# Performance work log

Measured on AMD Instinct MI355X. Metric: run time of the kernel, lower is better.

Reference implementation:

```python
import jax, jax.numpy as jnp
import numpy as np

# dims: 64 graphs x 1024 nodes, 32768 edges/graph, 256 feats, 64 pools/graph
B, NPG, EPG, F, C = 64, 1024, 32768, 256, 64
N, E = B * NPG, B * EPG


def setup_inputs() -> dict:
    key = jax.random.key(0)
    k1, k2, k3, k4, k5 = jax.random.split(key, 5)
    x = jax.random.normal(k1, (N, F), jnp.float32)
    # within-graph edges (block structure, as in real batched graphs)
    src = jax.random.randint(k2, (B, EPG), 0, NPG, dtype=jnp.int32)
    dst = jax.random.randint(k3, (B, EPG), 0, NPG, dtype=jnp.int32)
    off = (jnp.arange(B, dtype=jnp.int32) * NPG)[:, None]
    edge_index = jnp.stack([(src + off).reshape(-1), (dst + off).reshape(-1)], 0)
    edge_weight = jax.random.uniform(k4, (E,), jnp.float32)
    batch = jnp.repeat(jnp.arange(B, dtype=jnp.int32), NPG)
    batch_ptr = jnp.arange(B + 1, dtype=jnp.int32) * NPG
    # pooling_net stand-in: linear d_feat -> num_pools
    W = jax.random.normal(k5, (F, C), jnp.float32) * 0.05
    b = jnp.zeros((C,), jnp.float32)
    return dict(x=x, edge_index=edge_index, edge_weight=edge_weight,
                batch=batch, batch_ptr=batch_ptr, W=W, b=b)


def reference(x, edge_index, edge_weight, batch, batch_ptr, W, b):
    num_batches = batch_ptr.shape[0] - 1
    Cp = W.shape[1]  # num_pools_per_graph
    logits = x @ W + b                       # pooling_net(x, edge_index)
    sm = jax.nn.softmax(logits, axis=-1)     # [N, C]
    c = jnp.argmax(sm, axis=-1)              # hard cluster per node [N]
    p = jnp.take_along_axis(sm, c[:, None], axis=-1)[:, 0]
    # straight-through nonzero value of s (==1.0 in forward value)
    v = 1.0 - jax.lax.stop_gradient(p) + p
    gcl = batch * Cp + c                     # global cluster id [N]
    K = num_batches * Cp
    # out = S^T x  -> segment reduce over nodes by global cluster
    out = jax.ops.segment_sum(v[:, None] * x, gcl, num_segments=K)  # [K, F]
    # out_adj = S^T A S  (block diagonal over graphs): per-edge scatter
    src, dst = edge_index[0], edge_index[1]
    ci, cj = c[src], c[dst]
    gb = batch[src]
    flat = gb * (Cp * Cp) + ci * Cp + cj
    contrib = edge_weight * v[src] * v[dst]
    out_adj = jax.ops.segment_sum(contrib, flat, num_segments=num_batches * Cp * Cp)
    # dense block-diagonal index set (torch returns coalesced nonzeros;
    # jit needs static shapes, so we enumerate all within-graph pool pairs)
    idx = jnp.arange(num_batches * Cp * Cp, dtype=jnp.int32)
    bb, rem = idx // (Cp * Cp), idx % (Cp * Cp)
    out_edge_index = jnp.stack([bb * Cp + rem // Cp, bb * Cp + rem % Cp], 0)
    # link_loss = ||A - S S^T||_F / E  via exact decomposition
    a2 = jnp.sum(edge_weight * edge_weight)
    ap = jnp.sum(jnp.where(gcl[src] == gcl[dst], contrib, 0.0))
    vs2 = jax.ops.segment_sum(v * v, gcl, num_segments=K)
    p2 = jnp.sum(vs2 * vs2)
    link_loss = jnp.sqrt(jnp.maximum(a2 - 2.0 * ap + p2, 0.0)) / edge_index.shape[1]
    batch_out = jnp.repeat(jnp.arange(num_batches, dtype=jnp.int32), Cp)
    batch_ptr_out = jnp.arange(num_batches + 1, dtype=jnp.int32) * Cp
    return (out, out_edge_index, out_adj, link_loss, jnp.float32(0.0),
            batch_out, batch_ptr_out)
```

## Files before the change

### kernel.cpp

```cpp
#include <hip/hip_runtime.h>
#include <cstdint>
#include <cstddef>

typedef __attribute__((ext_vector_type(8))) short short8;
typedef __attribute__((ext_vector_type(4))) float f32x4;

#define GLOAD_LDS16(gsrc, ldst) \
    __builtin_amdgcn_global_load_lds( \
        (const __attribute__((address_space(1))) void*)(gsrc), \
        (__attribute__((address_space(3))) void*)(ldst), 16, 0, 0)

namespace {
constexpr int kN    = 65536;
constexpr int kF    = 256;
constexpr int kC    = 64;
constexpr int kNPG  = 1024;
constexpr int kB    = 64;
constexpr int kE    = 2097152;
constexpr int kK    = kB * kC;

constexpr size_t OFF_OUT  = 0;
constexpr size_t OFF_EIDX = (size_t)kK * kF;
constexpr size_t OFF_ADJ  = OFF_EIDX + 2ull*kB*kC*kC;
constexpr size_t OFF_LL   = OFF_ADJ + (size_t)kB*kC*kC;
constexpr size_t OFF_Z    = OFF_LL + 1;
constexpr size_t OFF_BOUT = OFF_Z + 1;
constexpr size_t OFF_BPTR = OFF_BOUT + kK;

constexpr size_t WS_C    = 0;
constexpr size_t WS_V    = 262144;
constexpr size_t WS_VS2  = 524288;
constexpr size_t WS_A2   = 540672;
constexpr size_t WS_PERM = 544768;
constexpr size_t WS_STRT = 806912;
constexpr size_t WS_WPH  = 1048576;
constexpr size_t WS_WPL  = 1081344;
constexpr size_t WS_PADJ = 544768;

__device__ __forceinline__ unsigned short bf16_rn(float f)
{
    const unsigned int b = __float_as_uint(f);
    return (unsigned short)((b + 0x7fffu + ((b >> 16) & 1u)) >> 16);
}
}

__global__ __launch_bounds__(256) void k_const(float* __restrict__ out,
                                               const float* __restrict__ Wm,
                                               unsigned short* __restrict__ wph,
                                               unsigned short* __restrict__ wpl)
{
    const int i = blockIdx.x * 256 + threadIdx.x;
    constexpr int E2 = 2 * kB * kC * kC;
    constexpr int B3 = E2 + kK + kB + 1;
    if (i < E2) {
        const int half = i >= kB*kC*kC;
        const int idx  = half ? i - kB*kC*kC : i;
        const int bb = idx >> 12, rem = idx & 4095;
        const int val = half ? bb*kC + (rem & 63) : bb*kC + (rem >> 6);
        out[OFF_EIDX + i] = (float)val;
    } else if (i < E2 + kK) {
        const int j = i - E2;
        out[OFF_BOUT + j] = (float)(j >> 6);
    } else if (i < B3) {
        const int j = i - (E2 + kK);
        out[OFF_BPTR + j] = (float)(j * kC);
    } else if (i < B3 + 32768) {
        const int j  = (i - B3) & 16383;
        const int lo = (i - B3) >= 16384;
        const int jj = j & 7, lane = (j >> 3) & 63;
        const int nt = (j >> 9) & 3, ks = j >> 11;
        const float wv = Wm[(size_t)(ks*32 + (lane>>4)*8 + jj)*kC
                            + nt*16 + (lane & 15)];
        const unsigned short h = bf16_rn(wv);
        if (!lo) {
            wph[j] = h;
        } else {
            const float hf = __uint_as_float((unsigned int)h << 16);
            wpl[j] = bf16_rn(wv - hf);
        }
    }
}

__global__ __launch_bounds__(256) void k_logits(
    const float* __restrict__ x, const unsigned short* __restrict__ wph,
    const unsigned short* __restrict__ wpl, const float* __restrict__ bv,
    int* __restrict__ carr, float* __restrict__ varr)
{
    __shared__ float xs[2][128 * 32];
    const int tid  = threadIdx.x;
    const int lane = tid & 63;
    const int w    = tid >> 6;
    const int nbase = blockIdx.x * 128;
    const int l15  = lane & 15;
    const int kgrp = lane >> 4;

    const int snode = lane >> 3;
    const int sfo   = (((lane & 7) ^ snode)) * 4;

    f32x4 acc[2][4];
#pragma unroll
    for (int mt = 0; mt < 2; ++mt)
#pragma unroll
        for (int nt = 0; nt < 4; ++nt)
            acc[mt][nt] = f32x4{0.f, 0.f, 0.f, 0.f};

#pragma unroll
    for (int i = 0; i < 4; ++i) {
        const int g = w*4 + i;
        const float* src = x + (size_t)(nbase + g*8 + snode)*kF + sfo;
        GLOAD_LDS16(src, &xs[0][g*256]);
    }

#pragma unroll 1
    for (int c = 0; c < 8; ++c) {
        if (c < 7) {
#pragma unroll
            for (int i = 0; i < 4; ++i) {
                const int g = w*4 + i;
                const float* src = x + (size_t)(nbase + g*8 + snode)*kF
                                     + (c+1)*32 + sfo;
                GLOAD_LDS16(src, &xs[(c+1) & 1][g*256]);
            }
            asm volatile("s_waitcnt vmcnt(4)" ::: "memory");
        } else {
            asm volatile("s_waitcnt vmcnt(0)" ::: "memory");
        }
        __syncthreads();

        const float* __restrict__ xb = &xs[c & 1][0];
        short8 bh[4], bl[4];
#pragma unroll
        for (int nt = 0; nt < 4; ++nt) {
            const size_t wo = ((size_t)(c*4 + nt)*64 + lane) * 8;
            bh[nt] = *reinterpret_cast<const short8*>(wph + wo);
            bl[nt] = *reinterpret_cast<const short8*>(wpl + wo);
        }
#pragma unroll
        for (int mt = 0; mt < 2; ++mt) {
            const int row = w*32 + mt*16 + l15;
            const int sA  = ((kgrp*2)     ^ (row & 7)) * 4;
            const int sC  = ((kgrp*2 + 1) ^ (row & 7)) * 4;
            const float4 xa = *reinterpret_cast<const float4*>(
                &xb[row*32 + sA]);
            const float4 xc = *reinterpret_cast<const float4*>(
                &xb[row*32 + sC]);
            const float xv[8] = {xa.x, xa.y, xa.z, xa.w,
                                 xc.x, xc.y, xc.z, xc.w};
            short8 ah, al;
#pragma unroll
            for (int j = 0; j < 8; ++j) {
                const unsigned short h = bf16_rn(xv[j]);
                const float hf = __uint_as_float((unsigned int)h << 16);
                ah[j] = (short)h;
                al[j] = (short)bf16_rn(xv[j] - hf);
            }
#pragma unroll
            for (int nt = 0; nt < 4; ++nt) {
                acc[mt][nt] = __builtin_amdgcn_mfma_f32_16x16x32_bf16(
                    ah, bh[nt], acc[mt][nt], 0, 0, 0);
                acc[mt][nt] = __builtin_amdgcn_mfma_f32_16x16x32_bf16(
                    al, bh[nt], acc[mt][nt], 0, 0, 0);
                acc[mt][nt] = __builtin_amdgcn_mfma_f32_16x16x32_bf16(
                    ah, bl[nt], acc[mt][nt], 0, 0, 0);
                acc[mt][nt] = __builtin_amdgcn_mfma_f32_16x16x32_bf16(
                    al, bl[nt], acc[mt][nt], 0, 0, 0);
            }
        }
        __syncthreads();
    }

#pragma unroll
    for (int mt = 0; mt < 2; ++mt) {
#pragma unroll
        for (int nt = 0; nt < 4; ++nt) {
            const float b = bv[nt*16 + l15];
#pragma unroll
            for (int r = 0; r < 4; ++r) acc[mt][nt][r] += b;
        }
#pragma unroll
        for (int r = 0; r < 4; ++r) {
            float m = acc[mt][0][r]; int ci = l15;
#pragma unroll
            for (int nt = 1; nt < 4; ++nt) {
                if (acc[mt][nt][r] > m) { m = acc[mt][nt][r]; ci = nt*16 + l15; }
            }
#pragma unroll
            for (int off = 1; off < 16; off <<= 1) {
                const float om = __shfl_xor(m, off);
                const int   oc = __shfl_xor(ci, off);
                if (om > m || (om == m && oc < ci)) { m = om; ci = oc; }
            }
            float s = 0.f;
#pragma unroll
            for (int nt = 0; nt < 4; ++nt) s += expf(acc[mt][nt][r] - m);
#pragma unroll
            for (int off = 1; off < 16; off <<= 1) s += __shfl_xor(s, off);
            if (l15 == r) {
                const float p = 1.0f / s;
                const int n = nbase + w*32 + mt*16 + kgrp*4 + r;
                carr[n] = ci;
                varr[n] = (1.0f - p) + p;
            }
        }
    }
}

__global__ __launch_bounds__(1024) void k_sort(
    const int* __restrict__ carr, int* __restrict__ perm,
    int* __restrict__ startc)
{
    __shared__ int hist[16][64];
    __shared__ int startS[65];
    const int g = blockIdx.x;
    const int tid = threadIdx.x;
    const int w = tid >> 6, lane = tid & 63;
    const int c = carr[g*kNPG + tid];
    hist[tid >> 6][tid & 63] = 0;
    __syncthreads();
    unsigned long long mm = ~0ull;
#pragma unroll
    for (int b = 0; b < 6; ++b) {
        const unsigned long long bal = __ballot((c >> b) & 1);
        mm &= ((c >> b) & 1) ? bal : ~bal;
    }
    const unsigned long long ltmask =
        (lane == 0) ? 0ull : (~0ull >> (64 - lane));
    const int rank_in_wave = __popcll(mm & ltmask);
    const int leader = __ffsll((unsigned long long)mm) - 1;
    if (lane == leader) hist[w][c] = __popcll(mm);
    __syncthreads();
    if (w == 0) {
        int tot = 0;
#pragma unroll
        for (int i = 0; i < 16; ++i) tot += hist[i][lane];
        int pre = tot;
#pragma unroll
        for (int off = 1; off < 64; off <<= 1) {
            const int t = __shfl_up(pre, off);
            if (lane >= off) pre += t;
        }
        startS[lane + 1] = pre;
        if (lane == 0) startS[0] = 0;
    }
    __syncthreads();
    int before = startS[c];
    for (int i = 0; i < w; ++i) before += hist[i][c];
    perm[g*kNPG + before + rank_in_wave] = g*kNPG + tid;
    if (tid < 65) startc[g*65 + tid] = startS[tid];
}

__global__ __launch_bounds__(1024) void k_pool_x(
    const float* __restrict__ x, const int* __restrict__ perm,
    const int* __restrict__ startc, const float* __restrict__ varr,
    float* __restrict__ out, float* __restrict__ vs2)
{
    const int tid  = threadIdx.x;
    const int g    = blockIdx.x >> 3;
    const int fh   = blockIdx.x & 7;
    const int w    = tid >> 6;
    const int lane = tid & 63;
    const int q    = lane & 7;
    const int sub  = lane >> 3;
    const int fbase = fh*32 + q*4;
#pragma unroll
    for (int cc = 0; cc < 4; ++cc) {
        const int c = w*4 + cc;
        const int s = startc[g*65 + c];
        const int e = startc[g*65 + c + 1];
        float ax = 0.f, ay = 0.f, az = 0.f, aw = 0.f, v2 = 0.f;
        for (int base = s + sub; base < e; base += 8) {
            const int n = perm[(size_t)g*kNPG + base];
            const float v = varr[n];
            const float4 xv = *reinterpret_cast<const float4*>(
                x + (size_t)n*kF + fbase);
            ax = fmaf(v, xv.x, ax); ay = fmaf(v, xv.y, ay);
            az = fmaf(v, xv.z, az); aw = fmaf(v, xv.w, aw);
            v2 = fmaf(v, v, v2);
        }
#pragma unroll
        for (int off = 8; off < 64; off <<= 1) {
            ax += __shfl_xor(ax, off); ay += __shfl_xor(ay, off);
            az += __shfl_xor(az, off); aw += __shfl_xor(aw, off);
            v2 += __shfl_xor(v2, off);
        }
        if (sub == 0) {
            const float4 o = {ax, ay, az, aw};
            *reinterpret_cast<float4*>(
                out + OFF_OUT + (size_t)(g*kC + c)*kF + fbase) = o;
        }
        if (fh == 0 && lane == 0) vs2[g*kC + c] = v2;
    }
}

__global__ __launch_bounds__(1024) void k_adj(
    const int* __restrict__ ei, const float* __restrict__ ew,
    const int* __restrict__ carr, const float* __restrict__ varr,
    float* __restrict__ padj, float* __restrict__ a2p)
{
    __shared__ float adj[kC*kC];
    __shared__ float vls[kNPG];
    __shared__ int   cls[kNPG];
    __shared__ float wred[16];
    const int tid = threadIdx.x;
    const int bid = blockIdx.x;
    const int g   = bid >> 3;
    for (int i = tid; i < kC*kC; i += 1024) adj[i] = 0.f;
    vls[tid] = varr[g*kNPG + tid];
    cls[tid] = carr[g*kNPG + tid];
    __syncthreads();
    const int e0 = bid * 4096;
    float a2l = 0.f;
#pragma unroll
    for (int it = 0; it < 4; ++it) {
        const int e  = e0 + it*1024 + tid;
        const int sn = ei[e]      & (kNPG - 1);
        const int dn = ei[kE + e] & (kNPG - 1);
        const float wv = ew[e];
        a2l += wv * wv;
        atomicAdd(&adj[cls[sn]*kC + cls[dn]], wv * vls[sn] * vls[dn]);
    }
    __syncthreads();
#pragma unroll
    for (int r = 0; r < 4; ++r) {
        const int lin = r*1024 + tid;
        padj[(size_t)bid*4096 + lin] = adj[lin];
    }
#pragma unroll
    for (int off = 32; off > 0; off >>= 1) a2l += __shfl_down(a2l, off);
    if ((tid & 63) == 0) wred[tid >> 6] = a2l;
    __syncthreads();
    if (tid == 0) {
        float s = 0.f;
#pragma unroll
        for (int wv = 0; wv < 16; ++wv) s += wred[wv];
        a2p[bid] = s;
    }
}

__global__ __launch_bounds__(256) void k_adj_merge(
    const float* __restrict__ padj, float* __restrict__ out)
{
    const int id = blockIdx.x*256 + threadIdx.x;
    const int g = id >> 12, idx = id & 4095;
    float s = 0.f;
#pragma unroll
    for (int sp = 0; sp < 8; ++sp) s += padj[(size_t)(g*8 + sp)*4096 + idx];
    out[OFF_ADJ + id] = s;
}

__global__ __launch_bounds__(256) void k_final(
    const float* __restrict__ vs2, const float* __restrict__ a2p,
    float* __restrict__ out)
{
    const int tid = threadIdx.x;
    float p2l = 0.f, apl = 0.f;
#pragma unroll
    for (int r = 0; r < 16; ++r) {
        const int k = r*256 + tid;
        const float t = vs2[k];
        p2l += t*t;
        const int g = k >> 6, cc = k & 63;
        apl += out[OFF_ADJ + (size_t)g*4096 + cc*65];
    }
    float a2l = a2p[tid] + a2p[tid + 256];
#pragma unroll
    for (int off = 32; off > 0; off >>= 1) {
        p2l += __shfl_down(p2l, off);
        apl += __shfl_down(apl, off);
        a2l += __shfl_down(a2l, off);
    }
    __shared__ float red[3][4];
    if ((tid & 63) == 0) {
        red[0][tid>>6] = p2l; red[1][tid>>6] = apl; red[2][tid>>6] = a2l;
    }
    __syncthreads();
    if (tid == 0) {
        const float p2 = red[0][0]+red[0][1]+red[0][2]+red[0][3];
        const float ap = red[1][0]+red[1][1]+red[1][2]+red[1][3];
        const float a2 = red[2][0]+red[2][1]+red[2][2]+red[2][3];
        const float val = a2 - 2.0f*ap + p2;
        out[OFF_LL] = sqrtf(fmaxf(val, 0.f)) / (float)kE;
        out[OFF_Z]  = 0.0f;
    }
}

extern "C" void kernel_launch(void* const* d_in, const int* in_sizes, int n_in,
                              void* d_out, int out_size, void* d_ws, size_t ws_size,
                              hipStream_t stream)
{
    const float* x  = (const float*)d_in[0];
    const int*   ei = (const int*)d_in[1];
    const float* ew = (const float*)d_in[2];
    const float* Wm = (const float*)d_in[5];
    const float* bv = (const float*)d_in[6];
    float* out = (float*)d_out;
    char*  ws  = (char*)d_ws;
    int*   carr  = (int*)(ws + WS_C);
    float* varr  = (float*)(ws + WS_V);
    float* vs2   = (float*)(ws + WS_VS2);
    float* a2p   = (float*)(ws + WS_A2);
    int*   perm  = (int*)(ws + WS_PERM);
    int*   strt  = (int*)(ws + WS_STRT);
    unsigned short* wph = (unsigned short*)(ws + WS_WPH);
    unsigned short* wpl = (unsigned short*)(ws + WS_WPL);
    float* padj  = (float*)(ws + WS_PADJ);

    k_const    <<<2193, 256, 0, stream>>>(out, Wm, wph, wpl);
    k_logits   <<<512,  256, 0, stream>>>(x, wph, wpl, bv, carr, varr);
    k_sort     <<<64,  1024, 0, stream>>>(carr, perm, strt);
    k_pool_x   <<<512, 1024, 0, stream>>>(x, perm, strt, varr, out, vs2);
    k_adj      <<<512, 1024, 0, stream>>>(ei, ew, carr, varr, padj, a2p);
    k_adj_merge<<<1024, 256, 0, stream>>>(padj, out);
    k_final    <<<1,    256, 0, stream>>>(vs2, a2p, out);
}
```

Baseline: 75.55 us.

## Stage bf16 split weights in LDS and make logits tiles wave-private

The logits kernel now preloads the whole hi/lo bf16 weight matrix into shared memory once per block, instead of reading it from global memory every chunk. Each block handles 64 nodes, and each wave owns a private 16-row slice of the x tile, so the per-chunk block barriers are dropped and waits use only per-wave vmcnt. The grid doubles to 1024 blocks. The trade-off is about 80KB of LDS per block, which limits occupancy, plus a 64KB weight copy into LDS for every block.

```diff
diff --git a/kernel.cpp b/kernel.cpp
--- a/kernel.cpp
+++ b/kernel.cpp
@@ -86,121 +86,116 @@
     const unsigned short* __restrict__ wpl, const float* __restrict__ bv,
     int* __restrict__ carr, float* __restrict__ varr)
 {
-    __shared__ float xs[2][128 * 32];
+    __shared__ unsigned short wlds[32768];
+    __shared__ float xsl[2][64 * 32];
     const int tid  = threadIdx.x;
     const int lane = tid & 63;
     const int w    = tid >> 6;
-    const int nbase = blockIdx.x * 128;
+    const int nbase = blockIdx.x * 64;
     const int l15  = lane & 15;
     const int kgrp = lane >> 4;
 
     const int snode = lane >> 3;
-    const int sfo   = (((lane & 7) ^ snode)) * 4;
-
-    f32x4 acc[2][4];
-#pragma unroll
-    for (int mt = 0; mt < 2; ++mt)
-#pragma unroll
-        for (int nt = 0; nt < 4; ++nt)
-            acc[mt][nt] = f32x4{0.f, 0.f, 0.f, 0.f};
-
-#pragma unroll
-    for (int i = 0; i < 4; ++i) {
-        const int g = w*4 + i;
-        const float* src = x + (size_t)(nbase + g*8 + snode)*kF + sfo;
-        GLOAD_LDS16(src, &xs[0][g*256]);
-    }
+    const int sfo   = ((lane & 7) ^ snode) * 4;
+
+    f32x4 acc[4];
+#pragma unroll
+    for (int nt = 0; nt < 4; ++nt) acc[nt] = f32x4{0.f, 0.f, 0.f, 0.f};
+
+#pragma unroll
+    for (int t = 0; t < 8; ++t) {
+        GLOAD_LDS16(wph + ((size_t)t*256 + tid)*8,
+                    &wlds[(t*256 + w*64)*8]);
+        GLOAD_LDS16(wpl + ((size_t)t*256 + tid)*8,
+                    &wlds[16384 + (t*256 + w*64)*8]);
+    }
+#pragma unroll
+    for (int i = 0; i < 2; ++i) {
+        const float* src = x + (size_t)(nbase + w*16 + i*8 + snode)*kF + sfo;
+        GLOAD_LDS16(src, &xsl[0][(w*16 + i*8)*32]);
+    }
+    asm volatile("s_waitcnt vmcnt(0)" ::: "memory");
+    __syncthreads();
 
 #pragma unroll 1
     for (int c = 0; c < 8; ++c) {
         if (c < 7) {
 #pragma unroll
-            for (int i = 0; i < 4; ++i) {
-                const int g = w*4 + i;
-                const float* src = x + (size_t)(nbase + g*8 + snode)*kF
+            for (int i = 0; i < 2; ++i) {
+                const float* src = x + (size_t)(nbase + w*16 + i*8 + snode)*kF
                                      + (c+1)*32 + sfo;
-                GLOAD_LDS16(src, &xs[(c+1) & 1][g*256]);
+                GLOAD_LDS16(src, &xsl[(c+1) & 1][(w*16 + i*8)*32]);
             }
-            asm volatile("s_waitcnt vmcnt(4)" ::: "memory");
+            asm volatile("s_waitcnt vmcnt(2)" ::: "memory");
         } else {
             asm volatile("s_waitcnt vmcnt(0)" ::: "memory");
         }
-        __syncthreads();
-
-        const float* __restrict__ xb = &xs[c & 1][0];
+
+        const float* __restrict__ xb = &xsl[c & 1][0];
         short8 bh[4], bl[4];
 #pragma unroll
         for (int nt = 0; nt < 4; ++nt) {
-            const size_t wo = ((size_t)(c*4 + nt)*64 + lane) * 8;
-            bh[nt] = *reinterpret_cast<const short8*>(wph + wo);
-            bl[nt] = *reinterpret_cast<const short8*>(wpl + wo);
-        }
-#pragma unroll
-        for (int mt = 0; mt < 2; ++mt) {
-            const int row = w*32 + mt*16 + l15;
-            const int sA  = ((kgrp*2)     ^ (row & 7)) * 4;
-            const int sC  = ((kgrp*2 + 1) ^ (row & 7)) * 4;
-            const float4 xa = *reinterpret_cast<const float4*>(
-                &xb[row*32 + sA]);
-            const float4 xc = *reinterpret_cast<const float4*>(
-                &xb[row*32 + sC]);
-            const float xv[8] = {xa.x, xa.y, xa.z, xa.w,
-                                 xc.x, xc.y, xc.z, xc.w};
-            short8 ah, al;
-#pragma unroll
-            for (int j = 0; j < 8; ++j) {
-                const unsigned short h = bf16_rn(xv[j]);
-                const float hf = __uint_as_float((unsigned int)h << 16);
-                ah[j] = (short)h;
-                al[j] = (short)bf16_rn(xv[j] - hf);
-            }
-#pragma unroll
-            for (int nt = 0; nt < 4; ++nt) {
-                acc[mt][nt] = __builtin_amdgcn_mfma_f32_16x16x32_bf16(
-                    ah, bh[nt], acc[mt][nt], 0, 0, 0);
-                acc[mt][nt] = __builtin_amdgcn_mfma_f32_16x16x32_bf16(
-                    al, bh[nt], acc[mt][nt], 0, 0, 0);
-                acc[mt][nt] = __builtin_amdgcn_mfma_f32_16x16x32_bf16(
-                    ah, bl[nt], acc[mt][nt], 0, 0, 0);
-                acc[mt][nt] = __builtin_amdgcn_mfma_f32_16x16x32_bf16(
-                    al, bl[nt], acc[mt][nt], 0, 0, 0);
-            }
-        }
-        __syncthreads();
-    }
-
-#pragma unroll
-    for (int mt = 0; mt < 2; ++mt) {
+            const int wo = ((c*4 + nt)*64 + lane) * 8;
+            bh[nt] = *reinterpret_cast<const short8*>(&wlds[wo]);
+            bl[nt] = *reinterpret_cast<const short8*>(&wlds[16384 + wo]);
+        }
+        const int row = w*16 + l15;
+        const int sA  = ((kgrp*2)     ^ (l15 & 7)) * 4;
+        const int sC  = ((kgrp*2 + 1) ^ (l15 & 7)) * 4;
+        const float4 xa = *reinterpret_cast<const float4*>(&xb[row*32 + sA]);
+        const float4 xc = *reinterpret_cast<const float4*>(&xb[row*32 + sC]);
+        const float xv[8] = {xa.x, xa.y, xa.z, xa.w,
+                             xc.x, xc.y, xc.z, xc.w};
+        short8 ah, al;
+#pragma unroll
+        for (int j = 0; j < 8; ++j) {
+            const unsigned short h = bf16_rn(xv[j]);
+            const float hf = __uint_as_float((unsigned int)h << 16);
+            ah[j] = (short)h;
+            al[j] = (short)bf16_rn(xv[j] - hf);
+        }
 #pragma unroll
         for (int nt = 0; nt < 4; ++nt) {
-            const float b = bv[nt*16 + l15];
-#pragma unroll
-            for (int r = 0; r < 4; ++r) acc[mt][nt][r] += b;
-        }
-#pragma unroll
-        for (int r = 0; r < 4; ++r) {
-            float m = acc[mt][0][r]; int ci = l15;
-#pragma unroll
-            for (int nt = 1; nt < 4; ++nt) {
-                if (acc[mt][nt][r] > m) { m = acc[mt][nt][r]; ci = nt*16 + l15; }
-            }
-#pragma unroll
-            for (int off = 1; off < 16; off <<= 1) {
-                const float om = __shfl_xor(m, off);
-                const int   oc = __shfl_xor(ci, off);
-                if (om > m || (om == m && oc < ci)) { m = om; ci = oc; }
-            }
-            float s = 0.f;
-#pragma unroll
-            for (int nt = 0; nt < 4; ++nt) s += expf(acc[mt][nt][r] - m);
-#pragma unroll
-            for (int off = 1; off < 16; off <<= 1) s += __shfl_xor(s, off);
-            if (l15 == r) {
-                const float p = 1.0f / s;
-                const int n = nbase + w*32 + mt*16 + kgrp*4 + r;
-                carr[n] = ci;
-                varr[n] = (1.0f - p) + p;
-            }
+            acc[nt] = __builtin_amdgcn_mfma_f32_16x16x32_bf16(
+                ah, bh[nt], acc[nt], 0, 0, 0);
+            acc[nt] = __builtin_amdgcn_mfma_f32_16x16x32_bf16(
+                al, bh[nt], acc[nt], 0, 0, 0);
+            acc[nt] = __builtin_amdgcn_mfma_f32_16x16x32_bf16(
+                ah, bl[nt], acc[nt], 0, 0, 0);
+            acc[nt] = __builtin_amdgcn_mfma_f32_16x16x32_bf16(
+                al, bl[nt], acc[nt], 0, 0, 0);
+        }
+    }
+
+#pragma unroll
+    for (int nt = 0; nt < 4; ++nt) {
+        const float b = bv[nt*16 + l15];
+#pragma unroll
+        for (int r = 0; r < 4; ++r) acc[nt][r] += b;
+    }
+#pragma unroll
+    for (int r = 0; r < 4; ++r) {
+        float m = acc[0][r]; int ci = l15;
+#pragma unroll
+        for (int nt = 1; nt < 4; ++nt) {
+            if (acc[nt][r] > m) { m = acc[nt][r]; ci = nt*16 + l15; }
+        }
+#pragma unroll
+        for (int off = 1; off < 16; off <<= 1) {
+            const float om = __shfl_xor(m, off);
+            const int   oc = __shfl_xor(ci, off);
+            if (om > m || (om == m && oc < ci)) { m = om; ci = oc; }
+        }
+        float s = 0.f;
+#pragma unroll
+        for (int nt = 0; nt < 4; ++nt) s += expf(acc[nt][r] - m);
+#pragma unroll
+        for (int off = 1; off < 16; off <<= 1) s += __shfl_xor(s, off);
+        if (l15 == r) {
+            const float p = 1.0f / s;
+            const int n = nbase + w*16 + kgrp*4 + r;
+            carr[n] = ci;
+            varr[n] = (1.0f - p) + p;
         }
     }
 }
@@ -406,7 +401,7 @@
     float* padj  = (float*)(ws + WS_PADJ);
 
     k_const    <<<2193, 256, 0, stream>>>(out, Wm, wph, wpl);
-    k_logits   <<<512,  256, 0, stream>>>(x, wph, wpl, bv, carr, varr);
+    k_logits   <<<1024, 256, 0, stream>>>(x, wph, wpl, bv, carr, varr);
     k_sort     <<<64,  1024, 0, stream>>>(carr, perm, strt);
     k_pool_x   <<<512, 1024, 0, stream>>>(x, perm, strt, varr, out, vs2);
     k_adj      <<<512, 1024, 0, stream>>>(ei, ew, carr, varr, padj, a2p);
```

New measurement: 76.49 us. No clear change (+1.2%).
